# Performance work log

Hardware: AMD Instinct MI355X
Metric: run time of the kernel (lower is better)

## Reference

```python
import jax, jax.numpy as jnp
import numpy as np

N_HEADS = 8

def setup_inputs() -> dict:
    key = jax.random.key(0)
    ks = jax.random.split(key, 7)
    B, S, D = 4, 2048, 512
    s = 1.0 / np.sqrt(D)
    return {
        "input_Q": jax.random.normal(ks[0], (B, S, D), jnp.float32),
        "input_K": jax.random.normal(ks[1], (B, S, D), jnp.float32),
        "input_V": jax.random.normal(ks[2], (B, S, D), jnp.float32),
        "W_Q": jax.random.normal(ks[3], (D, D), jnp.float32) * s,
        "W_K": jax.random.normal(ks[4], (D, D), jnp.float32) * s,
        "W_V": jax.random.normal(ks[5], (D, D), jnp.float32) * s,
        "W_O": jax.random.normal(ks[6], (D, D), jnp.float32) * s,
    }

def reference(input_Q, input_K, input_V, W_Q, W_K, W_V, W_O):
    B, Sq, D = input_Q.shape
    Sk = input_K.shape[1]
    H = N_HEADS
    d_k = D // H
    # torch nn.Linear(bias=False): y = x @ W.T
    def proj(x, W):
        return (x @ W.T).reshape(B, -1, H, d_k).transpose(0, 2, 1, 3)  # [B,H,S,dk]
    Q = proj(input_Q, W_Q)
    K = proj(input_K, W_K)
    V = proj(input_V, W_V)
    scale = 1.0 / jnp.sqrt(jnp.float32(d_k))
    scores = jnp.einsum("bhqd,bhkd->bhqk", Q, K) * scale  # [B,H,Sq,Sk]
    # TriangularCausalMask: mask strict upper triangle with -inf
    causal = jnp.tril(jnp.ones((Sq, Sk), dtype=bool))
    scores = jnp.where(causal[None, None], scores, -jnp.inf)
    attn = jax.nn.softmax(scores, axis=-1)
    context = jnp.einsum("bhqk,bhkd->bhqd", attn, V)
    context = context.transpose(0, 2, 1, 3).reshape(B, Sq, D)
    return context @ W_O.T
```

## Files before the change

kernel.cpp:

```cpp
#include <hip/hip_runtime.h>
#include <hip/hip_bf16.h>
#include <math.h>

#define B_  4
#define S_  2048
#define D_  512
#define H_  8
#define DK_ 64
#define M_  (B_ * S_)

using bf16   = __bf16;
using bf16x4 = __bf16 __attribute__((ext_vector_type(4)));
using bf16x8 = __bf16 __attribute__((ext_vector_type(8)));
using f32x4  = float __attribute__((ext_vector_type(4)));

#define MFMA16(a, b, c) __builtin_amdgcn_mfma_f32_16x16x32_bf16((a), (b), (c), 0, 0, 0)
#define EXP2(x) exp2f(x)

typedef __attribute__((address_space(3))) void       lds_void;
typedef const __attribute__((address_space(1))) void gbl_void;

__device__ __forceinline__ void async16(const bf16* g, bf16* lds) {
    __builtin_amdgcn_global_load_lds((gbl_void*)g, (lds_void*)lds, 16, 0, 0);
}

__device__ __forceinline__ bf16x8 ldg8(const bf16* p) {
    return *reinterpret_cast<const bf16x8*>(p);
}

__device__ __forceinline__ size_t fragbase(int g, int k0, int kk, int t) {
    return ((((size_t)(g * 8 + k0) * 2 + kk) * 4 + t) * 64) * 8;
}

__global__ __launch_bounds__(256) void cvt_all(
    const float* __restrict__ x0, const float* __restrict__ x1, const float* __restrict__ x2,
    const float* __restrict__ w0, const float* __restrict__ w1,
    const float* __restrict__ w2, const float* __restrict__ w3,
    bf16* __restrict__ dst)
{
    const int w    = blockIdx.x * 4 + (threadIdx.x >> 6);
    const int lane = threadIdx.x & 63;
    const int lg = lane >> 4, lc = lane & 15;
    const float* src;
    int c;
    size_t dbase;
    if (w < 24576) {
        const int seg = w >> 13;
        c = w & 8191;
        src = (seg == 0) ? x0 : (seg == 1) ? x1 : x2;
        dbase = (size_t)seg << 22;
    } else {
        const int jj = w - 24576;
        const int seg = jj >> 9;
        c = jj & 511;
        src = (seg == 0) ? w0 : (seg == 1) ? w1 : (seg == 2) ? w2 : w3;
        dbase = ((size_t)3 << 22) + ((size_t)seg << 18);
    }
    const int g = c >> 6, k0 = (c >> 3) & 7, kk = (c >> 2) & 1, t = c & 3;
    const size_t soff = ((size_t)(g * 64 + t * 16 + lc) << 9) + k0 * 64 + kk * 32 + lg * 8;
    f32x4 a = *reinterpret_cast<const f32x4*>(src + soff);
    f32x4 b = *reinterpret_cast<const f32x4*>(src + soff + 4);
    bf16x8 r;
    #pragma unroll
    for (int j = 0; j < 4; ++j) { r[j] = (bf16)a[j]; r[j + 4] = (bf16)b[j]; }
    *reinterpret_cast<bf16x8*>(dst + dbase + ((size_t)c << 9) + (size_t)lane * 8) = r;
}

__global__ __launch_bounds__(256) void gemm_qkv(
    const bf16* __restrict__ Xf, const bf16* __restrict__ Wf,
    bf16* __restrict__ qkv)
{
    const int bx  = blockIdx.x;
    const int xcd = bx & 7;
    const int idx = bx >> 3;
    const int mt  = xcd + 8 * (idx & 7);
    const int rest = idx >> 3;
    const int nt  = rest & 3;
    const int z   = rest >> 2;

    const bf16* Xz = Xf + (size_t)z * M_ * D_;
    const bf16* Wz = Wf + (size_t)z * D_ * D_;
    const bool vz = (z == 2);
    const bf16* A  = vz ? Xz : Wz;
    const bf16* Bm = vz ? Wz : Xz;

    const int lane = threadIdx.x & 63;
    const int wave = threadIdx.x >> 6;
    const int lc = lane & 15;
    const int lg = lane >> 4;
    const int gA = (vz ? 2 * mt : 2 * nt) + (wave >> 1);
    const int gB = (vz ? 2 * nt : 2 * mt) + (wave & 1);

    f32x4 acc[4][4] = {};

    #pragma unroll
    for (int k0 = 0; k0 < 8; ++k0) {
        #pragma unroll
        for (int kk = 0; kk < 2; ++kk) {
            bf16x8 af[4], bfm[4];
            #pragma unroll
            for (int t = 0; t < 4; ++t)
                af[t] = ldg8(A + fragbase(gA, k0, kk, t) + (size_t)lane * 8);
            #pragma unroll
            for (int t = 0; t < 4; ++t)
                bfm[t] = ldg8(Bm + fragbase(gB, k0, kk, t) + (size_t)lane * 8);
            #pragma unroll
            for (int mi = 0; mi < 4; ++mi)
                #pragma unroll
                for (int ni = 0; ni < 4; ++ni)
                    acc[mi][ni] = MFMA16(af[mi], bfm[ni], acc[mi][ni]);
        }
    }

    if (z < 2) {
        bf16* Y = qkv + (size_t)z * M_ * D_;
        const float sc = (z == 0) ? 0.125f * 1.4426950408889634f : 1.0f;
        #pragma unroll
        for (int mi = 0; mi < 4; ++mi)
            #pragma unroll
            for (int ni = 0; ni < 4; ++ni) {
                const int d = gA * 64 + mi * 16 + lg * 4;
                const int s = gB * 64 + ni * 16 + lc;
                bf16x4 v;
                #pragma unroll
                for (int r = 0; r < 4; ++r) v[r] = (bf16)(acc[mi][ni][r] * sc);
                const size_t oidx =
                    ((((size_t)(s >> 11) * H_ + (d >> 6)) * S_
                      + (s & (S_ - 1))) << 6) + (d & 63);
                *reinterpret_cast<bf16x4*>(&Y[oidx]) = v;
            }
    } else {
        bf16* Y = qkv + (size_t)2 * M_ * D_;
        #pragma unroll
        for (int mi = 0; mi < 4; ++mi)
            #pragma unroll
            for (int ni = 0; ni < 4; ++ni) {
                const int s = gA * 64 + mi * 16 + lg * 4;
                const int d = gB * 64 + ni * 16 + lc;
                bf16x4 v;
                #pragma unroll
                for (int r = 0; r < 4; ++r) v[r] = (bf16)acc[mi][ni][r];
                const size_t oidx =
                    ((((size_t)(s >> 11)) * H_ + (d >> 6)) << 17)
                    + (size_t)(d & 63) * S_ + (s & (S_ - 1));
                *reinterpret_cast<bf16x4*>(&Y[oidx]) = v;
            }
    }
}

__global__ __launch_bounds__(256) void gemm_out(
    const bf16* __restrict__ CtxF, const bf16* __restrict__ WoF,
    float* __restrict__ out)
{
    const int bx  = blockIdx.x;
    const int xcd = bx & 7;
    const int idx = bx >> 3;
    const int mt  = xcd + 8 * (idx & 15);
    const int nt  = idx >> 4;

    const int lane = threadIdx.x & 63;
    const int wave = threadIdx.x >> 6;
    const int lc = lane & 15;
    const int lg = lane >> 4;
    const int gA = 2 * nt + (wave >> 1);
    const int tA = (wave & 1) * 2;
    const int gB = mt;

    f32x4 acc[2][4] = {};

    #pragma unroll
    for (int k0 = 0; k0 < 8; ++k0) {
        #pragma unroll
        for (int kk = 0; kk < 2; ++kk) {
            bf16x8 af[2], bfm[4];
            #pragma unroll
            for (int ai = 0; ai < 2; ++ai)
                af[ai] = ldg8(WoF + fragbase(gA, k0, kk, tA + ai) + (size_t)lane * 8);
            #pragma unroll
            for (int t = 0; t < 4; ++t)
                bfm[t] = ldg8(CtxF + fragbase(gB, k0, kk, t) + (size_t)lane * 8);
            #pragma unroll
            for (int ai = 0; ai < 2; ++ai)
                #pragma unroll
                for (int ni = 0; ni < 4; ++ni)
                    acc[ai][ni] = MFMA16(af[ai], bfm[ni], acc[ai][ni]);
        }
    }

    #pragma unroll
    for (int ai = 0; ai < 2; ++ai)
        #pragma unroll
        for (int ni = 0; ni < 4; ++ni) {
            const int d = gA * 64 + (tA + ai) * 16 + lg * 4;
            const int s = gB * 64 + ni * 16 + lc;
            *reinterpret_cast<f32x4*>(&out[(size_t)s * D_ + d]) = acc[ai][ni];
        }
}

__device__ __forceinline__ bf16x8 pfrag(const f32x4 a, const f32x4 b) {
    union U4 { bf16x4 v; unsigned int u[2]; };
    U4 pa, pb;
    #pragma unroll
    for (int r = 0; r < 4; ++r) { pa.v[r] = (bf16)a[r]; pb.v[r] = (bf16)b[r]; }
    auto r0 = __builtin_amdgcn_permlane16_swap(pa.u[0], pb.u[0], false, false);
    auto r1 = __builtin_amdgcn_permlane16_swap(pa.u[1], pb.u[1], false, false);
    union U8 { unsigned int u[4]; bf16x8 v; } out;
    out.u[0] = r0[0]; out.u[1] = r1[0]; out.u[2] = r0[1]; out.u[3] = r1[1];
    return out.v;
}

__global__ __launch_bounds__(256) void attn(
    const bf16* __restrict__ QKV, bf16* __restrict__ CtxF)
{
    const int bx = blockIdx.x;
    const int bh = (bx & 7) * 4 + ((bx >> 3) & 3);
    const int pi = bx >> 5;
    const int b = bh >> 3, h = bh & 7;
    const size_t plane = (size_t)S_ * DK_;
    const bf16* Q  = QKV + (size_t)bh * plane;
    const bf16* Kp = QKV + (size_t)(B_ * H_) * plane + (size_t)bh * plane;
    const bf16* Vt = QKV + 2 * (size_t)(B_ * H_) * plane + (size_t)bh * plane;

    const int lane = threadIdx.x & 63;
    const int wave = threadIdx.x >> 6;
    const int lc = lane & 15;
    const int lg = lane >> 4;
    const int sg = ((lg & 1) << 1) | (lg >> 1);
    const int srow = wave * 16 + lc;
    const int mrow = wave * 16 + lc;

    __shared__ bf16 Ks[4][64 * 64];
    __shared__ bf16 Vs[4][64 * 64];

    const int lo = pi;
    const int hi = 31 - pi;

    const int qL = lo * 64 + mrow;
    const int qH = hi * 64 + mrow;
    bf16x8 qfL0 = ldg8(Q + (size_t)qL * DK_ + lg * 8);
    bf16x8 qfL1 = ldg8(Q + (size_t)qL * DK_ + 32 + lg * 8);
    bf16x8 qfH0 = ldg8(Q + (size_t)qH * DK_ + lg * 8);
    bf16x8 qfH1 = ldg8(Q + (size_t)qH * DK_ + 32 + lg * 8);

    f32x4 accL[4] = {}, accH[4] = {};
    float liL = 0.f, liH = 0.f;

    auto stage = [&](int n) {
        const int kn = n * 64;
        bf16* kd = Ks[n & 3];
        bf16* vd = Vs[n & 3];
        #pragma unroll
        for (int i = 0; i < 2; ++i) {
            const int kc  = i * 4 + lg;
            const int kcv = i * 4 + sg;
            async16(Kp + (size_t)(kn + srow) * DK_ + kc * 8,
                    kd + (i * 256 + wave * 64) * 8);
            async16(Vt + (size_t)srow * S_ + kn + kcv * 8,
                    vd + (i * 256 + wave * 64) * 8);
        }
    };

    stage(0); stage(1); stage(2);

    for (int j = 0; j <= hi; ++j) {
        if (j + 2 <= hi)      asm volatile("s_waitcnt vmcnt(8)" ::: "memory");
        else if (j + 1 <= hi) asm volatile("s_waitcnt vmcnt(4)" ::: "memory");
        else                  asm volatile("s_waitcnt vmcnt(0)" ::: "memory");
        __builtin_amdgcn_s_barrier();
        if (j + 3 <= hi) stage(j + 3);

        const bf16* ks = Ks[j & 3];
        const bf16* vs = Vs[j & 3];

        bf16x8 kf0[4], kf1[4], vf0[4], vf1[4];
        #pragma unroll
        for (int t = 0; t < 4; ++t) {
            kf0[t] = ldg8(&ks[(t * 64 + lane) * 8]);
            kf1[t] = ldg8(&ks[(256 + t * 64 + lane) * 8]);
            vf0[t] = ldg8(&vs[(t * 64 + lane) * 8]);
            vf1[t] = ldg8(&vs[(256 + t * 64 + lane) * 8]);
        }

        auto step = [&](const bf16x8& qf0, const bf16x8& qf1, bool diag,
                        f32x4* accO, float& li) {
            f32x4 st[4];
            #pragma unroll
            for (int t = 0; t < 4; ++t) {
                f32x4 zz = {};
                zz = MFMA16(kf0[t], qf0, zz);
                st[t] = MFMA16(kf1[t], qf1, zz);
            }
            float rs = 0.f;
            if (diag) {
                #pragma unroll
                for (int t = 0; t < 4; ++t)
                    #pragma unroll
                    for (int r = 0; r < 4; ++r) {
                        const int kl = t * 16 + lg * 4 + r;
                        const float pv = EXP2((kl <= mrow) ? st[t][r] : -1e30f);
                        st[t][r] = pv;
                        rs += pv;
                    }
            } else {
                #pragma unroll
                for (int t = 0; t < 4; ++t)
                    #pragma unroll
                    for (int r = 0; r < 4; ++r) {
                        const float pv = EXP2(st[t][r]);
                        st[t][r] = pv;
                        rs += pv;
                    }
            }
            li += rs;

            const bf16x8 p0 = pfrag(st[0], st[1]);
            const bf16x8 p1 = pfrag(st[2], st[3]);

            #pragma unroll
            for (int t = 0; t < 4; ++t) {
                accO[t] = MFMA16(vf0[t], p0, accO[t]);
                accO[t] = MFMA16(vf1[t], p1, accO[t]);
            }
        };

        step(qfH0, qfH1, j == hi, accH, liH);
        if (j <= lo) step(qfL0, qfL1, j == lo, accL, liL);
    }

    liL += __shfl_xor(liL, 16); liL += __shfl_xor(liL, 32);
    liH += __shfl_xor(liH, 16); liH += __shfl_xor(liH, 32);
    const float rlL = 1.0f / liL;
    const float rlH = 1.0f / liH;
    __syncthreads();
    bf16* T = &Ks[0][0] + wave * 1280;

    #pragma unroll
    for (int half = 0; half < 2; ++half) {
        const f32x4* accO = half ? accH : accL;
        const float rl = half ? rlH : rlL;
        const int jq = half ? hi : lo;
        #pragma unroll
        for (int t = 0; t < 4; ++t) {
            bf16x4 ov;
            #pragma unroll
            for (int r = 0; r < 4; ++r) ov[r] = (bf16)(accO[t][r] * rl);
            *reinterpret_cast<bf16x4*>(&T[lc * 72 + t * 16 + lg * 4]) = ov;
        }
        #pragma unroll
        for (int kk = 0; kk < 2; ++kk) {
            bf16x8 o8 = ldg8(&T[lc * 72 + kk * 32 + lg * 8]);
            *reinterpret_cast<bf16x8*>(
                &CtxF[fragbase(b * 32 + jq, h, kk, wave) + (size_t)lane * 8]) = o8;
        }
    }
}

extern "C" void kernel_launch(void* const* d_in, const int* in_sizes, int n_in,
                              void* d_out, int out_size, void* d_ws, size_t ws_size,
                              hipStream_t stream)
{
    float* out = (float*)d_out;

    bf16* Xf   = (bf16*)d_ws;
    bf16* Wf   = Xf + (size_t)3 * M_ * D_;
    bf16* qkv  = Wf + (size_t)4 * D_ * D_;
    bf16* ctxF = qkv + (size_t)3 * M_ * D_;

    cvt_all<<<6656, 256, 0, stream>>>(
        (const float*)d_in[0], (const float*)d_in[1], (const float*)d_in[2],
        (const float*)d_in[3], (const float*)d_in[4], (const float*)d_in[5],
        (const float*)d_in[6], Xf);

    gemm_qkv<<<dim3(768), 256, 0, stream>>>(Xf, Wf, qkv);
    attn<<<dim3(512), 256, 0, stream>>>(qkv, ctxF);
    gemm_out<<<dim3(512), 256, 0, stream>>>(ctxF, Wf + (size_t)3 * D_ * D_, out);
}
```

Measured before the change: 185.3 us.

## Split attention q-tile pair across two wave groups in 512-thread blocks

```diff
diff --git a/kernel.cpp b/kernel.cpp
--- a/kernel.cpp
+++ b/kernel.cpp
@@ -209,7 +209,7 @@
     return out.v;
 }
 
-__global__ __launch_bounds__(256) void attn(
+__global__ __launch_bounds__(512, 4) void attn(
     const bf16* __restrict__ QKV, bf16* __restrict__ CtxF)
 {
     const int bx = blockIdx.x;
@@ -223,66 +223,71 @@
 
     const int lane = threadIdx.x & 63;
     const int wave = threadIdx.x >> 6;
+    const int wv   = wave & 3;
+    const int half = wave >> 2;
     const int lc = lane & 15;
     const int lg = lane >> 4;
     const int sg = ((lg & 1) << 1) | (lg >> 1);
-    const int srow = wave * 16 + lc;
-    const int mrow = wave * 16 + lc;
+    const int srow = wv * 16 + lc;
+    const int mrow = wv * 16 + lc;
 
     __shared__ bf16 Ks[4][64 * 64];
     __shared__ bf16 Vs[4][64 * 64];
 
     const int lo = pi;
     const int hi = 31 - pi;
-
-    const int qL = lo * 64 + mrow;
-    const int qH = hi * 64 + mrow;
-    bf16x8 qfL0 = ldg8(Q + (size_t)qL * DK_ + lg * 8);
-    bf16x8 qfL1 = ldg8(Q + (size_t)qL * DK_ + 32 + lg * 8);
-    bf16x8 qfH0 = ldg8(Q + (size_t)qH * DK_ + lg * 8);
-    bf16x8 qfH1 = ldg8(Q + (size_t)qH * DK_ + 32 + lg * 8);
-
-    f32x4 accL[4] = {}, accH[4] = {};
-    float liL = 0.f, liH = 0.f;
+    const int myq = half ? lo : hi;
+
+    const int qR = myq * 64 + mrow;
+    bf16x8 qf0 = ldg8(Q + (size_t)qR * DK_ + lg * 8);
+    bf16x8 qf1 = ldg8(Q + (size_t)qR * DK_ + 32 + lg * 8);
+
+    f32x4 accO[4] = {};
+    float li = 0.f;
 
     auto stage = [&](int n) {
         const int kn = n * 64;
-        bf16* kd = Ks[n & 3];
-        bf16* vd = Vs[n & 3];
-        #pragma unroll
-        for (int i = 0; i < 2; ++i) {
-            const int kc  = i * 4 + lg;
-            const int kcv = i * 4 + sg;
-            async16(Kp + (size_t)(kn + srow) * DK_ + kc * 8,
-                    kd + (i * 256 + wave * 64) * 8);
-            async16(Vt + (size_t)srow * S_ + kn + kcv * 8,
-                    vd + (i * 256 + wave * 64) * 8);
+        if (half == 0) {
+            bf16* kd = Ks[n & 3];
+            #pragma unroll
+            for (int i = 0; i < 2; ++i) {
+                const int kc = i * 4 + lg;
+                async16(Kp + (size_t)(kn + srow) * DK_ + kc * 8,
+                        kd + (i * 256 + wv * 64) * 8);
+            }
+        } else {
+            bf16* vd = Vs[n & 3];
+            #pragma unroll
+            for (int i = 0; i < 2; ++i) {
+                const int kcv = i * 4 + sg;
+                async16(Vt + (size_t)srow * S_ + kn + kcv * 8,
+                        vd + (i * 256 + wv * 64) * 8);
+            }
         }
     };
 
     stage(0); stage(1); stage(2);
 
     for (int j = 0; j <= hi; ++j) {
-        if (j + 2 <= hi)      asm volatile("s_waitcnt vmcnt(8)" ::: "memory");
-        else if (j + 1 <= hi) asm volatile("s_waitcnt vmcnt(4)" ::: "memory");
+        if (j + 2 <= hi)      asm volatile("s_waitcnt vmcnt(4)" ::: "memory");
+        else if (j + 1 <= hi) asm volatile("s_waitcnt vmcnt(2)" ::: "memory");
         else                  asm volatile("s_waitcnt vmcnt(0)" ::: "memory");
         __builtin_amdgcn_s_barrier();
         if (j + 3 <= hi) stage(j + 3);
 
-        const bf16* ks = Ks[j & 3];
-        const bf16* vs = Vs[j & 3];
-
-        bf16x8 kf0[4], kf1[4], vf0[4], vf1[4];
-        #pragma unroll
-        for (int t = 0; t < 4; ++t) {
-            kf0[t] = ldg8(&ks[(t * 64 + lane) * 8]);
-            kf1[t] = ldg8(&ks[(256 + t * 64 + lane) * 8]);
-            vf0[t] = ldg8(&vs[(t * 64 + lane) * 8]);
-            vf1[t] = ldg8(&vs[(256 + t * 64 + lane) * 8]);
-        }
-
-        auto step = [&](const bf16x8& qf0, const bf16x8& qf1, bool diag,
-                        f32x4* accO, float& li) {
+        if (j <= myq) {
+            const bf16* ks = Ks[j & 3];
+            const bf16* vs = Vs[j & 3];
+
+            bf16x8 kf0[4], kf1[4], vf0[4], vf1[4];
+            #pragma unroll
+            for (int t = 0; t < 4; ++t) {
+                kf0[t] = ldg8(&ks[(t * 64 + lane) * 8]);
+                kf1[t] = ldg8(&ks[(256 + t * 64 + lane) * 8]);
+                vf0[t] = ldg8(&vs[(t * 64 + lane) * 8]);
+                vf1[t] = ldg8(&vs[(256 + t * 64 + lane) * 8]);
+            }
+
             f32x4 st[4];
             #pragma unroll
             for (int t = 0; t < 4; ++t) {
@@ -291,7 +296,7 @@
                 st[t] = MFMA16(kf1[t], qf1, zz);
             }
             float rs = 0.f;
-            if (diag) {
+            if (j == myq) {
                 #pragma unroll
                 for (int t = 0; t < 4; ++t)
                     #pragma unroll
@@ -321,37 +326,26 @@
                 accO[t] = MFMA16(vf0[t], p0, accO[t]);
                 accO[t] = MFMA16(vf1[t], p1, accO[t]);
             }
-        };
-
-        step(qfH0, qfH1, j == hi, accH, liH);
-        if (j <= lo) step(qfL0, qfL1, j == lo, accL, liL);
-    }
-
-    liL += __shfl_xor(liL, 16); liL += __shfl_xor(liL, 32);
-    liH += __shfl_xor(liH, 16); liH += __shfl_xor(liH, 32);
-    const float rlL = 1.0f / liL;
-    const float rlH = 1.0f / liH;
+        }
+    }
+
+    li += __shfl_xor(li, 16); li += __shfl_xor(li, 32);
+    const float rl = 1.0f / li;
     __syncthreads();
     bf16* T = &Ks[0][0] + wave * 1280;
 
     #pragma unroll
-    for (int half = 0; half < 2; ++half) {
-        const f32x4* accO = half ? accH : accL;
-        const float rl = half ? rlH : rlL;
-        const int jq = half ? hi : lo;
-        #pragma unroll
-        for (int t = 0; t < 4; ++t) {
-            bf16x4 ov;
-            #pragma unroll
-            for (int r = 0; r < 4; ++r) ov[r] = (bf16)(accO[t][r] * rl);
-            *reinterpret_cast<bf16x4*>(&T[lc * 72 + t * 16 + lg * 4]) = ov;
-        }
-        #pragma unroll
-        for (int kk = 0; kk < 2; ++kk) {
-            bf16x8 o8 = ldg8(&T[lc * 72 + kk * 32 + lg * 8]);
-            *reinterpret_cast<bf16x8*>(
-                &CtxF[fragbase(b * 32 + jq, h, kk, wave) + (size_t)lane * 8]) = o8;
-        }
+    for (int t = 0; t < 4; ++t) {
+        bf16x4 ov;
+        #pragma unroll
+        for (int r = 0; r < 4; ++r) ov[r] = (bf16)(accO[t][r] * rl);
+        *reinterpret_cast<bf16x4*>(&T[lc * 72 + t * 16 + lg * 4]) = ov;
+    }
+    #pragma unroll
+    for (int kk = 0; kk < 2; ++kk) {
+        bf16x8 o8 = ldg8(&T[lc * 72 + kk * 32 + lg * 8]);
+        *reinterpret_cast<bf16x8*>(
+            &CtxF[fragbase(b * 32 + myq, h, kk, wv) + (size_t)lane * 8]) = o8;
     }
 }
 
@@ -372,6 +366,6 @@
         (const float*)d_in[6], Xf);
 
     gemm_qkv<<<dim3(768), 256, 0, stream>>>(Xf, Wf, qkv);
-    attn<<<dim3(512), 256, 0, stream>>>(qkv, ctxF);
+    attn<<<dim3(512), 512, 0, stream>>>(qkv, ctxF);
     gemm_out<<<dim3(512), 256, 0, stream>>>(ctxF, Wf + (size_t)3 * D_ * D_, out);
 }
```

Result: faster. 174.7 us (-5.8%).
